# Kernel optimization log

Hardware: AMD Instinct MI355X
Metric: run time of the kernel (lower is better)

## Reference

```python
import jax, jax.numpy as jnp
import numpy as np

EPS = 1e-5

def conv2d(x, w, b=None, pad=1):
    y = jax.lax.conv_general_dilated(x, w, (1, 1), [(pad, pad), (pad, pad)],
                                     dimension_numbers=('NCHW', 'OIHW', 'NCHW'))
    if b is not None:
        y = y + b[None, :, None, None]
    return y

def batchnorm(x, g, b):
    m = x.mean((0, 2, 3), keepdims=True)
    v = x.var((0, 2, 3), keepdims=True)
    return g[None, :, None, None] * (x - m) * jax.lax.rsqrt(v + EPS) + b[None, :, None, None]

def local_conv(x, w12):
    # x: [B,Ci,H,W]; w12: [B,Ci*9,H,W] -> per-pixel depthwise 3x3 conv
    B, Ci, H, W = x.shape
    xp = jnp.pad(x, ((0, 0), (0, 0), (1, 1), (1, 1)))
    patches = jnp.stack([xp[:, :, dh:dh + H, dw:dw + W]
                         for dh in range(3) for dw in range(3)], axis=2)  # [B,Ci,9,H,W]
    return (patches * w12.reshape(B, Ci, 9, H, W)).sum(axis=2)

def setup_inputs() -> dict:
    key = jax.random.key(0)
    ks = jax.random.split(key, 20)
    B, Ci, Cw, H, W = 4, 64, 64, 128, 128
    s = 0.05
    return {
        'input': jax.random.normal(ks[0], (B, Ci, H, W), jnp.float32),
        'weight': jax.random.normal(ks[1], (B, Cw, H, W), jnp.float32),
        'w_conv11': jax.random.normal(ks[2], (Ci, Ci + Cw, 3, 3), jnp.float32) * s,
        'b_conv11': jnp.zeros((Ci,), jnp.float32),
        'w_conv12': jax.random.normal(ks[3], (Ci * 9, Ci, 3, 3), jnp.float32) * s,
        'b_conv12': jnp.zeros((Ci * 9,), jnp.float32),
        'w_conv21': jax.random.normal(ks[4], (Ci, Ci + Cw, 3, 3), jnp.float32) * s,
        'b_conv21': jnp.zeros((Ci,), jnp.float32),
        'w_conv22': jax.random.normal(ks[5], (Ci * Ci, Ci, 1, 1), jnp.float32) * s,
        'b_conv22': jnp.zeros((Ci * Ci,), jnp.float32),
        'local_bn_g': jnp.ones((Ci,), jnp.float32),
        'local_bn_b': jnp.zeros((Ci,), jnp.float32),
        'br_g': jnp.ones((Ci,), jnp.float32),
        'br_b': jnp.zeros((Ci,), jnp.float32),
        'w_conv3': jax.random.normal(ks[6], (Ci, Ci, 3, 3), jnp.float32) * s,
        'conv3_bn_g': jnp.ones((Ci,), jnp.float32),
        'conv3_bn_b': jnp.zeros((Ci,), jnp.float32),
    }

def reference(input, weight, w_conv11, b_conv11, w_conv12, b_conv12,
              w_conv21, b_conv21, w_conv22, b_conv22,
              local_bn_g, local_bn_b, br_g, br_b,
              w_conv3, conv3_bn_g, conv3_bn_b):
    B, Ci, H, W = input.shape
    cat = jnp.concatenate([input, weight], axis=1)
    w11 = jax.nn.relu(conv2d(cat, w_conv11, b_conv11))
    w12 = conv2d(w11, w_conv12, b_conv12)                      # [B,Ci*9,H,W]
    w21 = jax.nn.relu(conv2d(cat, w_conv21, b_conv21))
    pooled = w21.mean((2, 3), keepdims=True)                   # [B,Ci,1,1]
    w22 = conv2d(pooled, w_conv22, b_conv22, pad=0).reshape(B, Ci, Ci)
    out1 = jax.nn.relu(batchnorm(local_conv(input, w12), local_bn_g, local_bn_b))
    out2 = jnp.einsum('bij,bjn->bin', w22, out1.reshape(B, Ci, H * W)).reshape(B, Ci, H, W)
    out3 = jax.nn.relu(batchnorm(out2, br_g, br_b))
    out4 = jax.nn.relu(batchnorm(conv2d(out3, w_conv3, None), conv3_bn_g, conv3_bn_b))
    return out4
```

## Files before the change

### kernel.cpp

```cpp
#include <hip/hip_runtime.h>

#define EPSV 1e-5f
#define HP 130
#define HW 16384

typedef unsigned int u32;
typedef unsigned short bfu;
typedef __bf16 bf16x8 __attribute__((ext_vector_type(8)));
typedef float  f32x4  __attribute__((ext_vector_type(4)));

__device__ __forceinline__ bfu f2bf(float f){
  u32 u = __builtin_bit_cast(u32, f);
  return (bfu)((u + 0x7FFFu + ((u >> 16) & 1u)) >> 16);
}
__device__ __forceinline__ float bf2f(bfu h){
  return __builtin_bit_cast(float, ((u32)h) << 16);
}
__device__ __forceinline__ f32x4 mfma16(bf16x8 a, bf16x8 b, f32x4 c){
  return __builtin_amdgcn_mfma_f32_16x16x32_bf16(a, b, c, 0, 0, 0);
}
__device__ __forceinline__ bf16x8 ldsfrag(const bfu* p){
  return __builtin_bit_cast(bf16x8, *(const uint4*)p);
}


__global__ void k_zero_border(bfu* catT, bfu* w11T, bfu* out3T){
  int i = blockIdx.x*256 + threadIdx.x;
  if (i >= 4*516) return;
  int b = i/516, r = i - b*516;
  int hp, wpp;
  if (r < 130){ hp = 0; wpp = r; }
  else if (r < 260){ hp = 129; wpp = r - 130; }
  else { int r2 = r - 260; hp = 1 + (r2 >> 1); wpp = (r2 & 1)*129; }
  int pix = (b*HP + hp)*HP + wpp;
  uint4 z = {0,0,0,0};
  uint4* c4 = (uint4*)catT  + (size_t)pix*16;
  uint4* w4 = (uint4*)w11T  + (size_t)pix*8;
  uint4* o4 = (uint4*)out3T + (size_t)pix*8;
  #pragma unroll
  for (int k = 0; k < 16; ++k) c4[k] = z;
  #pragma unroll
  for (int k = 0; k < 8; ++k){ w4[k] = z; o4[k] = z; }
}

__global__ void k_prep_w(const float* __restrict__ w11w, const float* __restrict__ w21w,
                         const float* __restrict__ w12w, const float* __restrict__ w3w,
                         bfu* A11, bfu* A12, bfu* A3){
  const int total = 147456 + 331776 + 36864;
  for (int i = blockIdx.x*256 + threadIdx.x; i < total; i += gridDim.x*256){
    float v; bfu* dst;
    if (i < 147456){
      int tap = i >> 14, och = (i >> 7) & 127, cin = i & 127;
      v = (och < 64) ? w11w[(och*128 + cin)*9 + tap] : w21w[((och-64)*128 + cin)*9 + tap];
      dst = A11 + i;
    } else if (i < 147456 + 331776){
      int i2 = i - 147456;
      int g = i2 >> 12, t = g/9, tap2 = g%9;
      int c = (i2 >> 6) & 63, j = i2 & 63;
      v = w12w[((c*9 + t)*64 + j)*9 + tap2];
      dst = A12 + i2;
    } else {
      int i3 = i - (147456 + 331776);
      int tap2 = i3 >> 12, oc = (i3 >> 6) & 63, j = i3 & 63;
      v = w3w[(oc*64 + j)*9 + tap2];
      dst = A3 + i3;
    }
    *dst = f2bf(v);
  }
}

__global__ void k_prep_cat(const float* __restrict__ inp, const float* __restrict__ wgt, bfu* catT){
  __shared__ bfu lds[128*136];
  int b = blockIdx.y, h = blockIdx.x;
  int t = threadIdx.x;
  int w = t & 127, c0 = t >> 7;
  #pragma unroll 1
  for (int c = c0; c < 128; c += 2){
    const float* src = (c < 64) ? inp + ((b*64 + c)*128 + h)*128
                                : wgt + ((b*64 + (c-64))*128 + h)*128;
    lds[w*136 + c] = f2bf(src[w]);
  }
  __syncthreads();
  uint4* dst = (uint4*)catT;
  #pragma unroll
  for (int k = 0; k < 8; ++k){
    int idx = k*256 + t;
    int pix = idx >> 4, sub = idx & 15;
    uint4 v = *(const uint4*)&lds[pix*136 + sub*8];
    dst[(((b*HP + h+1)*HP) + (pix+1))*16 + sub] = v;
  }
}

__global__ __launch_bounds__(256) void k1_conv(
    const bfu* __restrict__ catT, const bfu* __restrict__ A11,
    const float* __restrict__ b11, const float* __restrict__ b21,
    bfu* __restrict__ w11T, float* __restrict__ poolP){
  __shared__ bfu lds[24480];
  int tid = threadIdx.x;
  int b = blockIdx.y, tile = blockIdx.x;
  int h0 = (tile >> 3)*8, w0 = (tile & 7)*16;

  const uint4* catT4 = (const uint4*)catT;
  for (int s = tid; s < 180*17; s += 256){
    int cell = s/17, sub = s%17;
    if (sub < 16){
      int th = cell/18, tw = cell%18;
      uint4 v = catT4[(((b*HP + h0+th)*HP) + (w0+tw))*16 + sub];
      *(uint4*)&lds[cell*136 + sub*8] = v;
    }
  }
  __syncthreads();

  int wid = tid >> 6, l = tid & 63, lg = l >> 4, pc = l & 15;
  int wm = wid >> 1, wn = wid & 1;
  f32x4 acc[4][4];
  #pragma unroll
  for (int i = 0; i < 4; ++i)
    #pragma unroll
    for (int j = 0; j < 4; ++j) acc[i][j] = f32x4{0.f,0.f,0.f,0.f};

  const uint4* A4 = (const uint4*)A11;
  #pragma unroll 3
  for (int tap = 0; tap < 9; ++tap){
    int kh = tap/3, kw = tap%3;
    #pragma unroll
    for (int jc = 0; jc < 4; ++jc){
      bf16x8 a[4], bb[4];
      #pragma unroll
      for (int fm = 0; fm < 4; ++fm){
        int row = wm*64 + fm*16 + pc;
        a[fm] = __builtin_bit_cast(bf16x8, A4[(tap*128 + row)*16 + jc*4 + lg]);
      }
      #pragma unroll
      for (int fn = 0; fn < 4; ++fn){
        int cell = (wn*4 + fn + kh)*18 + (pc + kw);
        bb[fn] = ldsfrag(&lds[cell*136 + jc*32 + lg*8]);
      }
      #pragma unroll
      for (int fm = 0; fm < 4; ++fm)
        #pragma unroll
        for (int fn = 0; fn < 4; ++fn)
          acc[fm][fn] = mfma16(a[fm], bb[fn], acc[fm][fn]);
    }
  }
  __syncthreads();

  if (wm == 0){
    #pragma unroll
    for (int fm = 0; fm < 4; ++fm)
      #pragma unroll
      for (int r = 0; r < 4; ++r){
        int och = fm*16 + lg*4 + r;
        float bias = b11[och];
        #pragma unroll
        for (int fn = 0; fn < 4; ++fn){
          float v = acc[fm][fn][r] + bias;
          v = v > 0.f ? v : 0.f;
          int px = wn*64 + fn*16 + pc;
          lds[px*72 + och] = f2bf(v);
        }
      }
  } else {
    float* statsF = (float*)&lds[20000];
    #pragma unroll
    for (int fm = 0; fm < 4; ++fm)
      #pragma unroll
      for (int r = 0; r < 4; ++r){
        int cw = fm*16 + lg*4 + r;
        float bias = b21[cw];
        float s = 0.f;
        #pragma unroll
        for (int fn = 0; fn < 4; ++fn){
          float v = acc[fm][fn][r] + bias;
          s += (v > 0.f ? v : 0.f);
        }
        s += __shfl_xor(s,1); s += __shfl_xor(s,2); s += __shfl_xor(s,4); s += __shfl_xor(s,8);
        if (pc == 0) statsF[wn*64 + cw] = s;
      }
  }
  __syncthreads();

  if (wid < 2){
    int px = tid;
    int h = h0 + (px >> 4), w = w0 + (px & 15);
    uint4* dst = (uint4*)w11T + (((b*HP + h+1)*HP) + (w+1))*8;
    const uint4* srcT = (const uint4*)&lds[px*72];
    #pragma unroll
    for (int k = 0; k < 8; ++k) dst[k] = srcT[k];
  }
  if (tid < 64){
    float* statsF = (float*)&lds[20000];
    poolP[(b*128 + tile)*64 + tid] = statsF[tid] + statsF[64 + tid];
  }
}

__global__ void k2a_pool(const float* __restrict__ poolP, float* pooled){
  int t = threadIdx.x;
  int b = t >> 6, c = t & 63;
  float s = 0.f;
  for (int tile = 0; tile < 128; ++tile) s += poolP[(b*128 + tile)*64 + c];
  pooled[t] = s * (1.f/16384.f);
}

__global__ void k2b_w22(const float* __restrict__ pooled, const float* __restrict__ W22,
                        const float* __restrict__ b22, bfu* __restrict__ w22bf){
  __shared__ float pl[64];
  int b = blockIdx.x >> 4, og = blockIdx.x & 15;
  if (threadIdx.x < 64) pl[threadIdx.x] = pooled[b*64 + threadIdx.x];
  __syncthreads();
  int o = og*256 + threadIdx.x;
  float acc = b22[o];
  #pragma unroll 4
  for (int c = 0; c < 64; ++c) acc += pl[c]*W22[o*64 + c];
  w22bf[b*4096 + o] = f2bf(acc);
}

__global__ __launch_bounds__(768, 3) void k3_fused(
    const bfu* __restrict__ w11T, const bfu* __restrict__ catT,
    const bfu* __restrict__ A12, const float* __restrict__ b12,
    float* __restrict__ out1, float* __restrict__ st1){
  __shared__ bfu ldsW[324*64];
  __shared__ float b12f[576];
  __shared__ f32x4 buf[1024];
  __shared__ float wp[512];
  int tid = threadIdx.x;
  int b = blockIdx.y, tile = blockIdx.x;
  int h0 = (tile >> 3)*16, w0 = (tile & 7)*16;

  const uint4* w11T4 = (const uint4*)w11T;
  for (int s = tid; s < 324*8; s += 768){
    int cell = s >> 3, sub = s & 7;
    int th = cell/18, tw = cell - th*18;
    uint4 v = w11T4[(((b*HP + h0+th)*HP) + (w0+tw))*8 + sub];
    *(uint4*)&ldsW[cell*64 + ((sub*8) ^ ((cell&7)<<3))] = v;
  }
  for (int i = tid; i < 576; i += 768) b12f[i] = b12[i];
  __syncthreads();

  int wid = tid >> 6, l = tid & 63, lg = l >> 4, pc = l & 15;
  int pg = wid & 3, g = wid >> 2;
  int w4 = pg*4;
  const uint4* A4 = (const uint4*)A12;
  f32x4 oacc[4][4];
  #pragma unroll
  for (int i = 0; i < 4; ++i)
    #pragma unroll
    for (int j = 0; j < 4; ++j) oacc[i][j] = f32x4{0.f,0.f,0.f,0.f};

  #pragma unroll 1
  for (int tl = 0; tl < 3; ++tl){
    int tt = g*3 + tl;
    f32x4 y[4][4];
    #pragma unroll
    for (int i = 0; i < 4; ++i)
      #pragma unroll
      for (int j = 0; j < 4; ++j) y[i][j] = f32x4{0.f,0.f,0.f,0.f};

    #pragma unroll 3
    for (int tap2 = 0; tap2 < 9; ++tap2){
      int s = tt*9 + tap2;
      int kh = tap2/3, kw = tap2 - kh*3;
      #pragma unroll
      for (int jc = 0; jc < 2; ++jc){
        bf16x8 a[4], bb[4];
        #pragma unroll
        for (int fm = 0; fm < 4; ++fm)
          a[fm] = __builtin_bit_cast(bf16x8, A4[s*512 + (fm*16 + pc)*8 + jc*4 + lg]);
        #pragma unroll
        for (int fn = 0; fn < 4; ++fn){
          int cell = (w4 + fn + kh)*18 + (pc + kw);
          bb[fn] = ldsfrag(&ldsW[cell*64 + ((jc*32 + lg*8) ^ ((cell&7)<<3))]);
        }
        #pragma unroll
        for (int fm = 0; fm < 4; ++fm)
          #pragma unroll
          for (int fn = 0; fn < 4; ++fn)
            y[fm][fn] = mfma16(a[fm], bb[fn], y[fm][fn]);
      }
    }

    int dh = tt/3, dw = tt - dh*3;
    #pragma unroll
    for (int fn = 0; fn < 4; ++fn){
      const bfu* base = catT + ((size_t)((b*HP + h0 + w4 + fn + dh)*HP) + (w0 + pc + dw))*128 + lg*4;
      #pragma unroll
      for (int fm = 0; fm < 4; ++fm){
        ushort4 iv = *(const ushort4*)(base + fm*16);
        float i0 = bf2f(iv.x), i1 = bf2f(iv.y), i2 = bf2f(iv.z), i3 = bf2f(iv.w);
        int c = fm*16 + lg*4;
        oacc[fm][fn][0] += i0 * (y[fm][fn][0] + b12f[(c+0)*9 + tt]);
        oacc[fm][fn][1] += i1 * (y[fm][fn][1] + b12f[(c+1)*9 + tt]);
        oacc[fm][fn][2] += i2 * (y[fm][fn][2] + b12f[(c+2)*9 + tt]);
        oacc[fm][fn][3] += i3 * (y[fm][fn][3] + b12f[(c+3)*9 + tt]);
      }
    }
  }

  #pragma unroll 1
  for (int fm = 0; fm < 4; ++fm){
    if (g == 2){
      #pragma unroll
      for (int fn = 0; fn < 4; ++fn)
        buf[((w4 + fn)*16 + pc)*4 + lg] = oacc[fm][fn];
    }
    __syncthreads();
    if (g == 1){
      #pragma unroll
      for (int fn = 0; fn < 4; ++fn){
        int idx = ((w4 + fn)*16 + pc)*4 + lg;
        f32x4 v = buf[idx];
        buf[idx] = v + oacc[fm][fn];
      }
    }
    __syncthreads();
    if (g == 0){
      f32x4 vv[4];
      #pragma unroll
      for (int fn = 0; fn < 4; ++fn)
        vv[fn] = buf[((w4 + fn)*16 + pc)*4 + lg] + oacc[fm][fn];
      #pragma unroll
      for (int r = 0; r < 4; ++r){
        int c = fm*16 + lg*4 + r;
        float s = 0.f, ss = 0.f;
        #pragma unroll
        for (int fn = 0; fn < 4; ++fn){
          float v = vv[fn][r];
          out1[((b*64 + c)*128 + h0 + w4 + fn)*128 + (w0 + pc)] = v;
          s += v; ss += v*v;
        }
        s += __shfl_xor(s,1); s += __shfl_xor(s,2); s += __shfl_xor(s,4); s += __shfl_xor(s,8);
        ss += __shfl_xor(ss,1); ss += __shfl_xor(ss,2); ss += __shfl_xor(ss,4); ss += __shfl_xor(ss,8);
        if (pc == 0){ wp[(pg*64 + c)*2] = s; wp[(pg*64 + c)*2 + 1] = ss; }
      }
    }
    __syncthreads();
  }
  if (tid < 64){
    float s = 0.f, ss = 0.f;
    #pragma unroll
    for (int w = 0; w < 4; ++w){ s += wp[(w*64 + tid)*2]; ss += wp[(w*64 + tid)*2 + 1]; }
    int blin = b*64 + tile;
    st1[(blin*64 + tid)*2] = s; st1[(blin*64 + tid)*2 + 1] = ss;
  }
}

__global__ void k_bnstat(const float* __restrict__ st, int nblk, float n,
                         const float* __restrict__ g, const float* __restrict__ bb, float* bn){
  __shared__ float red[512];
  int tid = threadIdx.x;
  int c = tid & 63, kk = tid >> 6;
  float s = 0.f, ss = 0.f;
  for (int k = kk; k < nblk; k += 4){
    float2 v = *(const float2*)&st[(k*64 + c)*2];
    s += v.x; ss += v.y;
  }
  red[tid*2] = s; red[tid*2 + 1] = ss;
  __syncthreads();
  if (tid < 64){
    #pragma unroll
    for (int q = 1; q < 4; ++q){ s += red[(q*64 + tid)*2]; ss += red[(q*64 + tid)*2 + 1]; }
    float mean = s/n, var = ss/n - mean*mean;
    float a = g[tid]*rsqrtf(var + EPSV);
    bn[tid*2] = a; bn[tid*2 + 1] = bb[tid] - mean*a;
  }
}

__global__ __launch_bounds__(256) void k4_einsum(
    const float* __restrict__ out1, const bfu* __restrict__ w22bf,
    const float* __restrict__ bn1, float* __restrict__ out2, float* __restrict__ st2){
  __shared__ bfu ldsX[256*72];
  __shared__ float a1[64], be1[64];
  __shared__ float wp[512];
  int tid = threadIdx.x;
  int b = blockIdx.y, chunk = blockIdx.x;
  if (tid < 64){ a1[tid] = bn1[tid*2]; be1[tid] = bn1[tid*2 + 1]; }
  __syncthreads();
  int p0 = chunk*256;

  {
    int px = tid;
    const float* src = out1 + (size_t)(b*64)*HW + p0 + px;
    #pragma unroll 1
    for (int j0 = 0; j0 < 64; j0 += 4){
      float x0 = src[(j0+0)*HW]; x0 = a1[j0+0]*x0 + be1[j0+0]; x0 = x0 > 0.f ? x0 : 0.f;
      float x1 = src[(j0+1)*HW]; x1 = a1[j0+1]*x1 + be1[j0+1]; x1 = x1 > 0.f ? x1 : 0.f;
      float x2 = src[(j0+2)*HW]; x2 = a1[j0+2]*x2 + be1[j0+2]; x2 = x2 > 0.f ? x2 : 0.f;
      float x3 = src[(j0+3)*HW]; x3 = a1[j0+3]*x3 + be1[j0+3]; x3 = x3 > 0.f ? x3 : 0.f;
      ushort4 pk; pk.x = f2bf(x0); pk.y = f2bf(x1); pk.z = f2bf(x2); pk.w = f2bf(x3);
      *(ushort4*)&ldsX[px*72 + j0] = pk;
    }
  }
  __syncthreads();

  int wid = tid >> 6, l = tid & 63, lg = l >> 4, pc = l & 15;
  const uint4* W4 = (const uint4*)w22bf;
  f32x4 acc[4][4];
  #pragma unroll
  for (int i = 0; i < 4; ++i)
    #pragma unroll
    for (int j = 0; j < 4; ++j) acc[i][j] = f32x4{0.f,0.f,0.f,0.f};

  #pragma unroll
  for (int jc = 0; jc < 2; ++jc){
    bf16x8 a[4], bb[4];
    #pragma unroll
    for (int fm = 0; fm < 4; ++fm)
      a[fm] = __builtin_bit_cast(bf16x8, W4[b*512 + (fm*16 + pc)*8 + jc*4 + lg]);
    #pragma unroll
    for (int fn = 0; fn < 4; ++fn)
      bb[fn] = ldsfrag(&ldsX[(wid*64 + fn*16 + pc)*72 + jc*32 + lg*8]);
    #pragma unroll
    for (int fm = 0; fm < 4; ++fm)
      #pragma unroll
      for (int fn = 0; fn < 4; ++fn)
        acc[fm][fn] = mfma16(a[fm], bb[fn], acc[fm][fn]);
  }

  #pragma unroll
  for (int fm = 0; fm < 4; ++fm)
    #pragma unroll
    for (int r = 0; r < 4; ++r){
      int i = fm*16 + lg*4 + r;
      float s = 0.f, ss = 0.f;
      #pragma unroll
      for (int fn = 0; fn < 4; ++fn){
        int px = wid*64 + fn*16 + pc;
        float v = acc[fm][fn][r];
        out2[(b*64 + i)*HW + p0 + px] = v;
        s += v; ss += v*v;
      }
      s += __shfl_xor(s,1); s += __shfl_xor(s,2); s += __shfl_xor(s,4); s += __shfl_xor(s,8);
      ss += __shfl_xor(ss,1); ss += __shfl_xor(ss,2); ss += __shfl_xor(ss,4); ss += __shfl_xor(ss,8);
      if (pc == 0){ wp[(wid*64 + i)*2] = s; wp[(wid*64 + i)*2 + 1] = ss; }
    }
  __syncthreads();
  if (tid < 64){
    float s = 0.f, ss = 0.f;
    #pragma unroll
    for (int w = 0; w < 4; ++w){ s += wp[(w*64 + tid)*2]; ss += wp[(w*64 + tid)*2 + 1]; }
    int blin = b*64 + chunk;
    st2[(blin*64 + tid)*2] = s; st2[(blin*64 + tid)*2 + 1] = ss;
  }
}

__global__ void k4c_out3(const float* __restrict__ out2, const float* __restrict__ bn2, bfu* out3T){
  __shared__ bfu lds[128*72];
  int b = blockIdx.y, h = blockIdx.x;
  int t = threadIdx.x;
  int px = t & 127, ch = (t >> 7)*32;
  #pragma unroll 1
  for (int cc = 0; cc < 32; cc += 4){
    int c = ch + cc;
    float x0 = out2[((b*64 + c+0) << 14) + (h << 7) + px];
    float x1 = out2[((b*64 + c+1) << 14) + (h << 7) + px];
    float x2 = out2[((b*64 + c+2) << 14) + (h << 7) + px];
    float x3 = out2[((b*64 + c+3) << 14) + (h << 7) + px];
    x0 = bn2[(c+0)*2]*x0 + bn2[(c+0)*2+1]; x0 = x0 > 0.f ? x0 : 0.f;
    x1 = bn2[(c+1)*2]*x1 + bn2[(c+1)*2+1]; x1 = x1 > 0.f ? x1 : 0.f;
    x2 = bn2[(c+2)*2]*x2 + bn2[(c+2)*2+1]; x2 = x2 > 0.f ? x2 : 0.f;
    x3 = bn2[(c+3)*2]*x3 + bn2[(c+3)*2+1]; x3 = x3 > 0.f ? x3 : 0.f;
    ushort4 pk; pk.x = f2bf(x0); pk.y = f2bf(x1); pk.z = f2bf(x2); pk.w = f2bf(x3);
    *(ushort4*)&lds[px*72 + c] = pk;
  }
  __syncthreads();
  uint4* dst = (uint4*)out3T;
  #pragma unroll
  for (int k = 0; k < 4; ++k){
    int idx = k*256 + t;
    int pix = idx >> 3, sub = idx & 7;
    uint4 v = *(const uint4*)&lds[pix*72 + sub*8];
    dst[((size_t)(b*HP + h+1)*HP + (pix+1))*8 + sub] = v;
  }
}

__global__ __launch_bounds__(256) void k5_conv3(
    const bfu* __restrict__ out3T, const bfu* __restrict__ A3,
    float* __restrict__ outc, float* __restrict__ st3){
  __shared__ bfu lds[180*72];
  __shared__ float wp[512];
  int tid = threadIdx.x;
  int b = blockIdx.y, tile = blockIdx.x;
  int h0 = (tile >> 3)*8, w0 = (tile & 7)*16;
  const uint4* src4 = (const uint4*)out3T;
  for (int s = tid; s < 180*8; s += 256){
    int cell = s >> 3, sub = s & 7;
    int th = cell/18, tw = cell - th*18;
    *(uint4*)&lds[cell*72 + sub*8] = src4[(((b*HP + h0+th)*HP) + (w0+tw))*8 + sub];
  }
  __syncthreads();

  int wid = tid >> 6, l = tid & 63, lg = l >> 4, pc = l & 15;
  f32x4 acc[4][2];
  #pragma unroll
  for (int i = 0; i < 4; ++i){ acc[i][0] = f32x4{0.f,0.f,0.f,0.f}; acc[i][1] = f32x4{0.f,0.f,0.f,0.f}; }
  const uint4* A4 = (const uint4*)A3;
  #pragma unroll 3
  for (int tap2 = 0; tap2 < 9; ++tap2){
    int kh = tap2/3, kw = tap2 - kh*3;
    #pragma unroll
    for (int jc = 0; jc < 2; ++jc){
      bf16x8 a[4], bb[2];
      #pragma unroll
      for (int fm = 0; fm < 4; ++fm)
        a[fm] = __builtin_bit_cast(bf16x8, A4[tap2*512 + (fm*16 + pc)*8 + jc*4 + lg]);
      #pragma unroll
      for (int fn = 0; fn < 2; ++fn){
        int cell = (wid*2 + fn + kh)*18 + (pc + kw);
        bb[fn] = ldsfrag(&lds[cell*72 + jc*32 + lg*8]);
      }
      #pragma unroll
      for (int fm = 0; fm < 4; ++fm)
        #pragma unroll
        for (int fn = 0; fn < 2; ++fn)
          acc[fm][fn] = mfma16(a[fm], bb[fn], acc[fm][fn]);
    }
  }
  #pragma unroll
  for (int fm = 0; fm < 4; ++fm)
    #pragma unroll
    for (int r = 0; r < 4; ++r){
      int c = fm*16 + lg*4 + r;
      float s = 0.f, ss = 0.f;
      #pragma unroll
      for (int fn = 0; fn < 2; ++fn){
        int pr = wid*2 + fn;
        float v = acc[fm][fn][r];
        outc[((b*64 + c)*128 + h0 + pr)*128 + (w0 + pc)] = v;
        s += v; ss += v*v;
      }
      s += __shfl_xor(s,1); s += __shfl_xor(s,2); s += __shfl_xor(s,4); s += __shfl_xor(s,8);
      ss += __shfl_xor(ss,1); ss += __shfl_xor(ss,2); ss += __shfl_xor(ss,4); ss += __shfl_xor(ss,8);
      if (pc == 0){ wp[(wid*64 + c)*2] = s; wp[(wid*64 + c)*2 + 1] = ss; }
    }
  __syncthreads();
  if (tid < 64){
    float s = 0.f, ss = 0.f;
    #pragma unroll
    for (int w = 0; w < 4; ++w){ s += wp[(w*64 + tid)*2]; ss += wp[(w*64 + tid)*2 + 1]; }
    int blin = b*128 + tile;
    st3[(blin*64 + tid)*2] = s; st3[(blin*64 + tid)*2 + 1] = ss;
  }
}

__global__ void k6_final(float4* __restrict__ out, const float* __restrict__ bn3){
  const int total4 = 4*64*HW/4;
  for (int i = blockIdx.x*256 + threadIdx.x; i < total4; i += gridDim.x*256){
    int c = (i >> 12) & 63;
    float a = bn3[c*2], be = bn3[c*2 + 1];
    float4 x = out[i];
    x.x = a*x.x + be; x.x = x.x > 0.f ? x.x : 0.f;
    x.y = a*x.y + be; x.y = x.y > 0.f ? x.y : 0.f;
    x.z = a*x.z + be; x.z = x.z > 0.f ? x.z : 0.f;
    x.w = a*x.w + be; x.w = x.w > 0.f ? x.w : 0.f;
    out[i] = x;
  }
}

extern "C" void kernel_launch(void* const* d_in, const int* in_sizes, int n_in,
                              void* d_out, int out_size, void* d_ws, size_t ws_size,
                              hipStream_t stream){
  const float* inp  = (const float*)d_in[0];
  const float* wgt  = (const float*)d_in[1];
  const float* w11w = (const float*)d_in[2];
  const float* b11  = (const float*)d_in[3];
  const float* w12w = (const float*)d_in[4];
  const float* b12  = (const float*)d_in[5];
  const float* w21w = (const float*)d_in[6];
  const float* b21  = (const float*)d_in[7];
  const float* W22  = (const float*)d_in[8];
  const float* b22  = (const float*)d_in[9];
  const float* lg   = (const float*)d_in[10];
  const float* lb   = (const float*)d_in[11];
  const float* brg  = (const float*)d_in[12];
  const float* brb  = (const float*)d_in[13];
  const float* w3w  = (const float*)d_in[14];
  const float* c3g  = (const float*)d_in[15];
  const float* c3b  = (const float*)d_in[16];

  if (ws_size < 53200000) return;

  char* ws = (char*)d_ws;
  bfu*   catT  = (bfu*)(ws);
  bfu*   w11T  = (bfu*)(ws + 17305600);
  bfu*   out3T = (bfu*)(ws + 25958400);
  bfu*   A11   = (bfu*)(ws + 34611200);
  bfu*   A12   = (bfu*)(ws + 34906112);
  bfu*   A3    = (bfu*)(ws + 35569664);
  float* out1  = (float*)(ws + 35643392);
  float* poolP = (float*)(ws + 52420608);
  float* pooled= (float*)(ws + 52551680);
  bfu*   w22bf = (bfu*)(ws + 52552704);
  float* st1   = (float*)(ws + 52585472);
  float* bn1   = (float*)(ws + 52716544);
  float* st2   = (float*)(ws + 52717056);
  float* bn2   = (float*)(ws + 52848128);
  float* st3   = (float*)(ws + 52848640);
  float* bn3   = (float*)(ws + 53110784);
  float* outF  = (float*)d_out;

  k_zero_border<<<dim3(9),  dim3(256), 0, stream>>>(catT, w11T, out3T);
  k_prep_w  <<<dim3(512),  dim3(256), 0, stream>>>(w11w, w21w, w12w, w3w, A11, A12, A3);
  k_prep_cat<<<dim3(128,4),dim3(256), 0, stream>>>(inp, wgt, catT);
  k1_conv   <<<dim3(128,4),dim3(256), 0, stream>>>(catT, A11, b11, b21, w11T, poolP);
  k2a_pool  <<<dim3(1),    dim3(256), 0, stream>>>(poolP, pooled);
  k2b_w22   <<<dim3(64),   dim3(256), 0, stream>>>(pooled, W22, b22, w22bf);
  k3_fused  <<<dim3(64,4), dim3(768), 0, stream>>>(w11T, catT, A12, b12, out1, st1);
  k_bnstat  <<<dim3(1),    dim3(256), 0, stream>>>(st1, 256, 65536.f, lg, lb, bn1);
  k4_einsum <<<dim3(64,4), dim3(256), 0, stream>>>(out1, w22bf, bn1, outF, st2);
  k_bnstat  <<<dim3(1),    dim3(256), 0, stream>>>(st2, 256, 65536.f, brg, brb, bn2);
  k4c_out3  <<<dim3(128,4),dim3(256), 0, stream>>>(outF, bn2, out3T);
  k5_conv3  <<<dim3(128,4),dim3(256), 0, stream>>>(out3T, A3, outF, st3);
  k_bnstat  <<<dim3(1),    dim3(256), 0, stream>>>(st3, 512, 65536.f, c3g, c3b, bn3);
  k6_final  <<<dim3(1024), dim3(256), 0, stream>>>((float4*)outF, bn3);
}
```

Before: 333.9 us.

## Restructure k3_fused into smaller 8x16 tiles with 4 waves looping all taps

The fused local-conv kernel drops from 768-thread blocks that split the 9 outer taps across three wave groups and reduced partial sums through LDS with several barriers. It now uses 256-thread blocks over 8x16 pixel tiles, and each wave covers all 9 taps for two rows, so the cross-group LDS reduction and its syncs go away. The grid doubles to 512 blocks, which gives more blocks to spread across the CUs, and the stats buffer is shared with conv3. In exchange each block reloads its A12 fragments and a 10-row halo for half the pixels, which raises weight traffic per output.

```diff
diff --git a/kernel.cpp b/kernel.cpp
--- a/kernel.cpp
+++ b/kernel.cpp
@@ -215,46 +215,39 @@
   w22bf[b*4096 + o] = f2bf(acc);
 }
 
-__global__ __launch_bounds__(768, 3) void k3_fused(
+__global__ __launch_bounds__(256) void k3_fused(
     const bfu* __restrict__ w11T, const bfu* __restrict__ catT,
     const bfu* __restrict__ A12, const float* __restrict__ b12,
     float* __restrict__ out1, float* __restrict__ st1){
-  __shared__ bfu ldsW[324*64];
+  __shared__ bfu ldsW[180*64];
   __shared__ float b12f[576];
-  __shared__ f32x4 buf[1024];
   __shared__ float wp[512];
   int tid = threadIdx.x;
   int b = blockIdx.y, tile = blockIdx.x;
-  int h0 = (tile >> 3)*16, w0 = (tile & 7)*16;
+  int h0 = (tile >> 3)*8, w0 = (tile & 7)*16;
 
   const uint4* w11T4 = (const uint4*)w11T;
-  for (int s = tid; s < 324*8; s += 768){
+  for (int s = tid; s < 180*8; s += 256){
     int cell = s >> 3, sub = s & 7;
     int th = cell/18, tw = cell - th*18;
     uint4 v = w11T4[(((b*HP + h0+th)*HP) + (w0+tw))*8 + sub];
     *(uint4*)&ldsW[cell*64 + ((sub*8) ^ ((cell&7)<<3))] = v;
   }
-  for (int i = tid; i < 576; i += 768) b12f[i] = b12[i];
+  for (int i = tid; i < 576; i += 256) b12f[i] = b12[i];
   __syncthreads();
 
   int wid = tid >> 6, l = tid & 63, lg = l >> 4, pc = l & 15;
-  int pg = wid & 3, g = wid >> 2;
-  int w4 = pg*4;
+  int w2 = wid*2;
   const uint4* A4 = (const uint4*)A12;
-  f32x4 oacc[4][4];
-  #pragma unroll
-  for (int i = 0; i < 4; ++i)
-    #pragma unroll
-    for (int j = 0; j < 4; ++j) oacc[i][j] = f32x4{0.f,0.f,0.f,0.f};
+  f32x4 oacc[4][2];
+  #pragma unroll
+  for (int i = 0; i < 4; ++i){ oacc[i][0] = f32x4{0.f,0.f,0.f,0.f}; oacc[i][1] = f32x4{0.f,0.f,0.f,0.f}; }
 
   #pragma unroll 1
-  for (int tl = 0; tl < 3; ++tl){
-    int tt = g*3 + tl;
-    f32x4 y[4][4];
-    #pragma unroll
-    for (int i = 0; i < 4; ++i)
-      #pragma unroll
-      for (int j = 0; j < 4; ++j) y[i][j] = f32x4{0.f,0.f,0.f,0.f};
+  for (int tt = 0; tt < 9; ++tt){
+    f32x4 y[4][2];
+    #pragma unroll
+    for (int i = 0; i < 4; ++i){ y[i][0] = f32x4{0.f,0.f,0.f,0.f}; y[i][1] = f32x4{0.f,0.f,0.f,0.f}; }
 
     #pragma unroll 3
     for (int tap2 = 0; tap2 < 9; ++tap2){
@@ -262,27 +255,27 @@
       int kh = tap2/3, kw = tap2 - kh*3;
       #pragma unroll
       for (int jc = 0; jc < 2; ++jc){
-        bf16x8 a[4], bb[4];
+        bf16x8 a[4], bb[2];
         #pragma unroll
         for (int fm = 0; fm < 4; ++fm)
           a[fm] = __builtin_bit_cast(bf16x8, A4[s*512 + (fm*16 + pc)*8 + jc*4 + lg]);
         #pragma unroll
-        for (int fn = 0; fn < 4; ++fn){
-          int cell = (w4 + fn + kh)*18 + (pc + kw);
+        for (int fn = 0; fn < 2; ++fn){
+          int cell = (w2 + fn + kh)*18 + (pc + kw);
           bb[fn] = ldsfrag(&ldsW[cell*64 + ((jc*32 + lg*8) ^ ((cell&7)<<3))]);
         }
         #pragma unroll
         for (int fm = 0; fm < 4; ++fm)
           #pragma unroll
-          for (int fn = 0; fn < 4; ++fn)
+          for (int fn = 0; fn < 2; ++fn)
             y[fm][fn] = mfma16(a[fm], bb[fn], y[fm][fn]);
       }
     }
 
     int dh = tt/3, dw = tt - dh*3;
     #pragma unroll
-    for (int fn = 0; fn < 4; ++fn){
-      const bfu* base = catT + ((size_t)((b*HP + h0 + w4 + fn + dh)*HP) + (w0 + pc + dw))*128 + lg*4;
+    for (int fn = 0; fn < 2; ++fn){
+      const bfu* base = catT + ((size_t)((b*HP + h0 + w2 + fn + dh)*HP) + (w0 + pc + dw))*128 + lg*4;
       #pragma unroll
       for (int fm = 0; fm < 4; ++fm){
         ushort4 iv = *(const ushort4*)(base + fm*16);
@@ -296,50 +289,28 @@
     }
   }
 
-  #pragma unroll 1
-  for (int fm = 0; fm < 4; ++fm){
-    if (g == 2){
-      #pragma unroll
-      for (int fn = 0; fn < 4; ++fn)
-        buf[((w4 + fn)*16 + pc)*4 + lg] = oacc[fm][fn];
-    }
-    __syncthreads();
-    if (g == 1){
-      #pragma unroll
-      for (int fn = 0; fn < 4; ++fn){
-        int idx = ((w4 + fn)*16 + pc)*4 + lg;
-        f32x4 v = buf[idx];
-        buf[idx] = v + oacc[fm][fn];
-      }
-    }
-    __syncthreads();
-    if (g == 0){
-      f32x4 vv[4];
-      #pragma unroll
-      for (int fn = 0; fn < 4; ++fn)
-        vv[fn] = buf[((w4 + fn)*16 + pc)*4 + lg] + oacc[fm][fn];
-      #pragma unroll
-      for (int r = 0; r < 4; ++r){
-        int c = fm*16 + lg*4 + r;
-        float s = 0.f, ss = 0.f;
-        #pragma unroll
-        for (int fn = 0; fn < 4; ++fn){
-          float v = vv[fn][r];
-          out1[((b*64 + c)*128 + h0 + w4 + fn)*128 + (w0 + pc)] = v;
-          s += v; ss += v*v;
-        }
-        s += __shfl_xor(s,1); s += __shfl_xor(s,2); s += __shfl_xor(s,4); s += __shfl_xor(s,8);
-        ss += __shfl_xor(ss,1); ss += __shfl_xor(ss,2); ss += __shfl_xor(ss,4); ss += __shfl_xor(ss,8);
-        if (pc == 0){ wp[(pg*64 + c)*2] = s; wp[(pg*64 + c)*2 + 1] = ss; }
-      }
-    }
-    __syncthreads();
-  }
+  #pragma unroll
+  for (int fm = 0; fm < 4; ++fm)
+    #pragma unroll
+    for (int r = 0; r < 4; ++r){
+      int c = fm*16 + lg*4 + r;
+      float s = 0.f, ss = 0.f;
+      #pragma unroll
+      for (int fn = 0; fn < 2; ++fn){
+        float v = oacc[fm][fn][r];
+        out1[((b*64 + c)*128 + h0 + w2 + fn)*128 + (w0 + pc)] = v;
+        s += v; ss += v*v;
+      }
+      s += __shfl_xor(s,1); s += __shfl_xor(s,2); s += __shfl_xor(s,4); s += __shfl_xor(s,8);
+      ss += __shfl_xor(ss,1); ss += __shfl_xor(ss,2); ss += __shfl_xor(ss,4); ss += __shfl_xor(ss,8);
+      if (pc == 0){ wp[(wid*64 + c)*2] = s; wp[(wid*64 + c)*2 + 1] = ss; }
+    }
+  __syncthreads();
   if (tid < 64){
     float s = 0.f, ss = 0.f;
     #pragma unroll
     for (int w = 0; w < 4; ++w){ s += wp[(w*64 + tid)*2]; ss += wp[(w*64 + tid)*2 + 1]; }
-    int blin = b*64 + tile;
+    int blin = b*128 + tile;
     st1[(blin*64 + tid)*2] = s; st1[(blin*64 + tid)*2 + 1] = ss;
   }
 }
@@ -590,12 +561,11 @@
   float* poolP = (float*)(ws + 52420608);
   float* pooled= (float*)(ws + 52551680);
   bfu*   w22bf = (bfu*)(ws + 52552704);
-  float* st1   = (float*)(ws + 52585472);
-  float* bn1   = (float*)(ws + 52716544);
-  float* st2   = (float*)(ws + 52717056);
-  float* bn2   = (float*)(ws + 52848128);
-  float* st3   = (float*)(ws + 52848640);
-  float* bn3   = (float*)(ws + 53110784);
+  float* st13  = (float*)(ws + 52585472);
+  float* bn1   = (float*)(ws + 52847616);
+  float* st2   = (float*)(ws + 52848128);
+  float* bn2   = (float*)(ws + 52979200);
+  float* bn3   = (float*)(ws + 52979712);
   float* outF  = (float*)d_out;
 
   k_zero_border<<<dim3(9),  dim3(256), 0, stream>>>(catT, w11T, out3T);
@@ -604,12 +574,12 @@
   k1_conv   <<<dim3(128,4),dim3(256), 0, stream>>>(catT, A11, b11, b21, w11T, poolP);
   k2a_pool  <<<dim3(1),    dim3(256), 0, stream>>>(poolP, pooled);
   k2b_w22   <<<dim3(64),   dim3(256), 0, stream>>>(pooled, W22, b22, w22bf);
-  k3_fused  <<<dim3(64,4), dim3(768), 0, stream>>>(w11T, catT, A12, b12, out1, st1);
-  k_bnstat  <<<dim3(1),    dim3(256), 0, stream>>>(st1, 256, 65536.f, lg, lb, bn1);
+  k3_fused  <<<dim3(128,4),dim3(256), 0, stream>>>(w11T, catT, A12, b12, out1, st13);
+  k_bnstat  <<<dim3(1),    dim3(256), 0, stream>>>(st13, 512, 65536.f, lg, lb, bn1);
   k4_einsum <<<dim3(64,4), dim3(256), 0, stream>>>(out1, w22bf, bn1, outF, st2);
   k_bnstat  <<<dim3(1),    dim3(256), 0, stream>>>(st2, 256, 65536.f, brg, brb, bn2);
   k4c_out3  <<<dim3(128,4),dim3(256), 0, stream>>>(outF, bn2, out3T);
-  k5_conv3  <<<dim3(128,4),dim3(256), 0, stream>>>(out3T, A3, outF, st3);
-  k_bnstat  <<<dim3(1),    dim3(256), 0, stream>>>(st3, 512, 65536.f, c3g, c3b, bn3);
+  k5_conv3  <<<dim3(128,4),dim3(256), 0, stream>>>(out3T, A3, outF, st13);
+  k_bnstat  <<<dim3(1),    dim3(256), 0, stream>>>(st13, 512, 65536.f, c3g, c3b, bn3);
   k6_final  <<<dim3(1024), dim3(256), 0, stream>>>((float4*)outF, bn3);
 }
```

Result: slower. 385.2 us (+15.4%).
